# Performance work log

Measured on AMD Instinct MI355X. Metric: run time of the kernel, lower is better.

Reference implementation:

```python
import jax, jax.numpy as jnp
import numpy as np


def _lstm_layer(x, w_ih, w_hh, b_ih, b_hh):
    """Single LSTM layer, batch_first x: [B, T, D] -> [B, T, H]. Gate order i,f,g,o."""
    B, T, _ = x.shape
    H = w_hh.shape[1]
    # Precompute input-to-gates for all timesteps: [B, T, 4H]
    xg = jnp.einsum('btd,gd->btg', x, w_ih) + b_ih + b_hh

    def step(carry, xg_t):
        h, c = carry
        g = xg_t + h @ w_hh.T  # [B, 4H]
        i, f, gg, o = jnp.split(g, 4, axis=-1)
        i = jax.nn.sigmoid(i)
        f = jax.nn.sigmoid(f)
        gg = jnp.tanh(gg)
        o = jax.nn.sigmoid(o)
        c = f * c + i * gg
        h = o * jnp.tanh(c)
        return (h, c), h

    h0 = jnp.zeros((B, H), x.dtype)
    (_, _), hs = jax.lax.scan(step, (h0, h0), jnp.swapaxes(xg, 0, 1))
    return jnp.swapaxes(hs, 0, 1)  # [B, T, H]


def setup_inputs() -> dict:
    key = jax.random.key(0)
    ks = jax.random.split(key, 11)
    B, T, E, H = 128, 512, 256, 512
    s_e = 1.0 / np.sqrt(H)
    inp = {
        'x': jax.random.normal(ks[0], (B, T, E), jnp.float32),
        'w_ih0': jax.random.uniform(ks[1], (4 * H, E), jnp.float32, -s_e, s_e),
        'w_hh0': jax.random.uniform(ks[2], (4 * H, H), jnp.float32, -s_e, s_e),
        'b_ih0': jax.random.uniform(ks[3], (4 * H,), jnp.float32, -s_e, s_e),
        'b_hh0': jax.random.uniform(ks[4], (4 * H,), jnp.float32, -s_e, s_e),
        'w_ih1': jax.random.uniform(ks[5], (4 * H, H), jnp.float32, -s_e, s_e),
        'w_hh1': jax.random.uniform(ks[6], (4 * H, H), jnp.float32, -s_e, s_e),
        'b_ih1': jax.random.uniform(ks[7], (4 * H,), jnp.float32, -s_e, s_e),
        'b_hh1': jax.random.uniform(ks[8], (4 * H,), jnp.float32, -s_e, s_e),
        'w_fc': jax.random.uniform(ks[9], (1, H), jnp.float32, -s_e, s_e),
        'b_fc': jax.random.uniform(ks[10], (1,), jnp.float32, -s_e, s_e),
    }
    return inp


def reference(x, w_ih0, w_hh0, b_ih0, b_hh0, w_ih1, w_hh1, b_ih1, b_hh1, w_fc, b_fc):
    h1 = _lstm_layer(x, w_ih0, w_hh0, b_ih0, b_hh0)   # [B, T, H]
    h2 = _lstm_layer(h1, w_ih1, w_hh1, b_ih1, b_hh1)  # [B, T, H]
    last = h2[:, -1, :]                               # [B, H]
    out = last @ w_fc.T + b_fc                        # [B, 1]
    return jax.nn.sigmoid(out)
```

## Files before the change

kernel.cpp:

```cpp
#include <hip/hip_runtime.h>

using u16    = unsigned short;
using u64_t  = unsigned long long;
using short4v = __attribute__((ext_vector_type(4))) short;
using short8 = __attribute__((ext_vector_type(8))) short;
using f32x4  = __attribute__((ext_vector_type(4))) float;

#define T_STEPS 512
#define BATCH   128
#define HDIM    512
#define EDIM    256
#define NWG     256
#define WGS     256
#define HPITCH  65536

__device__ __forceinline__ u16 f2bf(float f) {
  unsigned u = __float_as_uint(f);
  u += 0x7FFFu + ((u >> 16) & 1u);
  return (u16)(u >> 16);
}
__device__ __forceinline__ float bf2f(u16 h) {
  return __uint_as_float(((unsigned)h) << 16);
}
__device__ __forceinline__ float sigm(float x) { return 1.0f / (1.0f + __expf(-x)); }
__device__ __forceinline__ float ftanh(float x) { return 1.0f - 2.0f / (__expf(2.0f * x) + 1.0f); }

__device__ __forceinline__ u64_t cl8(const u16* p) {
  return __hip_atomic_load((const u64_t*)p, __ATOMIC_RELAXED, __HIP_MEMORY_SCOPE_AGENT);
}
__device__ __forceinline__ void cstore2(u16* p, u16 v) {
  __hip_atomic_store(p, v, __ATOMIC_RELAXED, __HIP_MEMORY_SCOPE_AGENT);
}
__device__ __forceinline__ int ld4(const int* p) {
  return __hip_atomic_load(p, __ATOMIC_RELAXED, __HIP_MEMORY_SCOPE_AGENT);
}
__device__ __forceinline__ short8 mk8(u64_t lo, u64_t hi) {
  short4v a = __builtin_bit_cast(short4v, lo);
  short4v b = __builtin_bit_cast(short4v, hi);
  return __builtin_shufflevector(a, b, 0, 1, 2, 3, 4, 5, 6, 7);
}

__global__ void cvt_bf16_kernel(const float* __restrict__ src, u16* __restrict__ dst, int n4) {
  int i = blockIdx.x * blockDim.x + threadIdx.x;
  if (i >= n4) return;
  float4 v = ((const float4*)src)[i];
  uint2 o;
  o.x = (unsigned)f2bf(v.x) | ((unsigned)f2bf(v.y) << 16);
  o.y = (unsigned)f2bf(v.z) | ((unsigned)f2bf(v.w) << 16);
  ((uint2*)dst)[i] = o;
}


__device__ __forceinline__ void grid_barrier(int* cnt, int* root, int* rel,
                                             int it, int tid, int bid) {
  __syncthreads();
  if (tid == 0) {
    int* mycnt = cnt + (bid >> 5) * 64;
    int old = __hip_atomic_fetch_add(mycnt, 1, __ATOMIC_RELAXED, __HIP_MEMORY_SCOPE_AGENT);
    if (old == 32 * (it + 1) - 1) {
      int r = __hip_atomic_fetch_add(root, 1, __ATOMIC_RELAXED, __HIP_MEMORY_SCOPE_AGENT);
      if (r == 8 * (it + 1) - 1)
        __hip_atomic_store(rel, it + 1, __ATOMIC_RELAXED, __HIP_MEMORY_SCOPE_AGENT);
    }
    while (__hip_atomic_load(rel, __ATOMIC_RELAXED, __HIP_MEMORY_SCOPE_AGENT) < it + 1)
      __builtin_amdgcn_s_sleep(1);
  }
  __syncthreads();
}

__global__ void __launch_bounds__(WGS, 1) lstm_kernel(
    const float* __restrict__ wih0, const float* __restrict__ whh0,
    const float* __restrict__ bih0, const float* __restrict__ bhh0,
    const float* __restrict__ wih1, const float* __restrict__ whh1,
    const float* __restrict__ bih1, const float* __restrict__ bhh1,
    const float* __restrict__ wfc,  const float* __restrict__ bfc,
    const u16* __restrict__ xbf, u16* __restrict__ h0buf, u16* __restrict__ h1buf,
    float* __restrict__ out, int* syncp, int hist)
{
  extern __shared__ u16 smem[];
  u16* Ws_in  = smem;
  u16* Ws_rec = smem + 16384;

  const int tid    = threadIdx.x;
  const int bid    = blockIdx.x;
  const int layer  = bid >> 7;
  const int lb     = bid & 127;
  const int mhalf  = lb & 1;
  const int nc     = lb >> 1;
  const int jbase  = nc * 8;
  const int w      = tid >> 6;
  const int lane   = tid & 63;
  const int l15    = lane & 15;
  const int q      = lane >> 4;
  const int wmbase = mhalf * 64 + w * 16;
  const int gid    = layer * 2 + mhalf;

  char* sb = (char*)syncp;

  const int K_in = layer ? HDIM : EDIM;
  const float* Wih = layer ? wih1 : wih0;
  const float* Whh = layer ? whh1 : whh0;
  const float* Bih = layer ? bih1 : bih0;
  const float* Bhh = layer ? bhh1 : bhh0;

  for (int p = tid; p < 32 * (K_in / 8); p += WGS) {
    int c = p >> 5, n = p & 31;
    int grow = (n >> 3) * HDIM + jbase + (n & 7);
    const float* s = Wih + (size_t)grow * K_in + c * 8;
    u16* d = Ws_in + p * 8;
    #pragma unroll
    for (int e = 0; e < 8; ++e) d[e] = f2bf(s[e]);
  }
  for (int p = tid; p < 32 * (HDIM / 8); p += WGS) {
    int c = p >> 5, n = p & 31;
    int grow = (n >> 3) * HDIM + jbase + (n & 7);
    const float* s = Whh + (size_t)grow * HDIM + c * 8;
    u16* d = Ws_rec + p * 8;
    #pragma unroll
    for (int e = 0; e < 8; ++e) d[e] = f2bf(s[e]);
  }

  const int cc = l15 & 7;
  const float bi_i = Bih[0*HDIM + jbase + cc] + Bhh[0*HDIM + jbase + cc];
  const float bi_f = Bih[1*HDIM + jbase + cc] + Bhh[1*HDIM + jbase + cc];
  const float bi_g = Bih[2*HDIM + jbase + cc] + Bhh[2*HDIM + jbase + cc];
  const float bi_o = Bih[3*HDIM + jbase + cc] + Bhh[3*HDIM + jbase + cc];

  __syncthreads();

  float cst[4] = {0.f, 0.f, 0.f, 0.f};
  u16* ownbuf = layer ? h1buf : h0buf;
  const int arow = wmbase + l15;
  const size_t cbase = ((size_t)q * 128 + arow) * 8;

  auto MM2 = [&](short8 a, const u16* Ws, int kk, f32x4& A0, f32x4& A1) {
    const u16* bb = Ws + (kk * 4 + q) * 256 + l15 * 8;
    short8 b0 = *(const short8*)bb;
    short8 b1 = *(const short8*)(bb + 128);
    A0 = __builtin_amdgcn_mfma_f32_16x16x32_bf16(a, b0, A0, 0, 0, 0);
    A1 = __builtin_amdgcn_mfma_f32_16x16x32_bf16(a, b1, A1, 0, 0, 0);
  };

  if (hist) {
    const int* own_rel = (const int*)(sb + 20480 + (size_t)(gid * 8 + (nc >> 3)) * 256);
    const int* l0_rel  = (const int*)(sb + 20480 + (size_t)(mhalf * 8 + (nc >> 3)) * 256);
    int* sub_cnt = (int*)(sb + (size_t)gid * 4096 + (size_t)(nc >> 3) * 256);
    int* root_cnt = (int*)(sb + 16384 + (size_t)gid * 256);

    for (int t = 0; t < T_STEPS; ++t) {
      short8 xfr[8];
      if (layer == 0) {
        const u16* xb = xbf + ((size_t)arow * T_STEPS + t) * EDIM + q * 8;
        #pragma unroll
        for (int kk = 0; kk < 8; ++kk) xfr[kk] = *(const short8*)(xb + kk * 32);
      }

      if (tid == 0) {
        if (layer == 0) {
          if (t > 0) while (ld4(own_rel) < t) {}
        } else {
          while (ld4(own_rel) < t || ld4(l0_rel) < t + 1) {}
        }
      }
      __syncthreads();

      short8 ifr[16];
      short8 rfr[16];
      if (layer == 1) {
        const u16* ab = h0buf + (size_t)t * HPITCH + cbase;
        #pragma unroll
        for (int kk = 0; kk < 16; ++kk) ifr[kk] = *(const short8*)(ab + kk * 4096);
      }
      if (t > 0) {
        const u16* rb = ownbuf + (size_t)(t - 1) * HPITCH + cbase;
        #pragma unroll
        for (int kk = 0; kk < 16; ++kk) rfr[kk] = *(const short8*)(rb + kk * 4096);
      }

      f32x4 a0A = {0,0,0,0}, a1A = {0,0,0,0}, a0B = {0,0,0,0}, a1B = {0,0,0,0};
      if (layer == 0) {
        #pragma unroll
        for (int kk = 0; kk < 8; ++kk)
          MM2(xfr[kk], Ws_in, kk, (kk & 1) ? a0B : a0A, (kk & 1) ? a1B : a1A);
      } else {
        #pragma unroll
        for (int kk = 0; kk < 16; ++kk)
          MM2(ifr[kk], Ws_in, kk, (kk & 1) ? a0B : a0A, (kk & 1) ? a1B : a1A);
      }
      if (t > 0) {
        #pragma unroll
        for (int kk = 0; kk < 16; ++kk)
          MM2(rfr[kk], Ws_rec, kk, (kk & 1) ? a0B : a0A, (kk & 1) ? a1B : a1A);
      }
      f32x4 acc0 = a0A + a0B;
      f32x4 acc1 = a1A + a1B;

      u16* hw = ownbuf + (size_t)t * HPITCH + (size_t)nc * 1024;
      const bool low = (l15 < 8);
      #pragma unroll
      for (int r = 0; r < 4; ++r) {
        float a0 = acc0[r], a1 = acc1[r];
        float p0 = __shfl_xor(a0, 8);
        float p1 = __shfl_xor(a1, 8);
        float iv = low ? a0 : p0;
        float fv = low ? p0 : a0;
        float gv = low ? a1 : p1;
        float ov = low ? p1 : a1;
        iv = sigm(iv + bi_i);
        fv = sigm(fv + bi_f);
        gv = ftanh(gv + bi_g);
        ov = sigm(ov + bi_o);
        float cn = fv * cst[r] + iv * gv;
        cst[r] = cn;
        float hv = ov * ftanh(cn);
        if (low) cstore2(&hw[(size_t)(wmbase + q * 4 + r) * 8 + cc], f2bf(hv));
      }

      __syncthreads();
      if (tid == 0) {
        int old = __hip_atomic_fetch_add(sub_cnt, 1, __ATOMIC_RELAXED, __HIP_MEMORY_SCOPE_AGENT);
        if (old == 8 * (t + 1) - 1) {
          int r = __hip_atomic_fetch_add(root_cnt, 1, __ATOMIC_RELAXED, __HIP_MEMORY_SCOPE_AGENT);
          if (r == 8 * (t + 1) - 1) {
            #pragma unroll
            for (int l = 0; l < 8; ++l)
              __hip_atomic_store((int*)(sb + 20480 + (size_t)(gid * 8 + l) * 256), t + 1,
                                 __ATOMIC_RELAXED, __HIP_MEMORY_SCOPE_AGENT);
          }
        }
      }
    }

    if (bid == NWG - 1) {
      const int* g2 = (const int*)(sb + 20480 + (size_t)(2 * 8 + 0) * 256);
      const int* g3 = (const int*)(sb + 20480 + (size_t)(3 * 8 + 0) * 256);
      if (tid == 0) { while (ld4(g2) < T_STEPS || ld4(g3) < T_STEPS) {} }
      __syncthreads();
      __builtin_amdgcn_fence(__ATOMIC_ACQUIRE, "agent");
      const int b = tid >> 1, half = tid & 1;
      const u16* hp = h1buf + (size_t)(T_STEPS - 1) * HPITCH;
      const float* wf = wfc + half * 256;
      float s = 0.f;
      for (int cg = 0; cg < 32; ++cg) {
        const u16* p = hp + ((size_t)(half * 32 + cg) * 128 + b) * 8;
        #pragma unroll
        for (int e = 0; e < 8; ++e) s += bf2f(p[e]) * wf[cg * 8 + e];
      }
      s += __shfl_xor(s, 1);
      if (half == 0) out[b] = sigm(s + bfc[0]);
    }
    return;
  }

  int* f_cnt  = (int*)(sb + 28672);
  int* f_root = (int*)(sb + 30720);
  int* f_rel  = (int*)(sb + 30848);
  for (int it = 0; it <= T_STEPS; ++it) {
    const int t = layer ? (it - 1) : it;
    if (t >= 0 && t < T_STEPS) {
      short8 ifr[16];
      short8 rfr[16];
      short8 xfr[8];
      if (layer == 1) {
        const u16* ab = h0buf + (size_t)(t & 1) * HPITCH + cbase;
        #pragma unroll
        for (int kk = 0; kk < 16; ++kk)
          ifr[kk] = mk8(cl8(ab + kk * 4096), cl8(ab + kk * 4096 + 4));
      }
      if (t > 0) {
        const u16* rb = ownbuf + (size_t)((t - 1) & 1) * HPITCH + cbase;
        #pragma unroll
        for (int kk = 0; kk < 16; ++kk)
          rfr[kk] = mk8(cl8(rb + kk * 4096), cl8(rb + kk * 4096 + 4));
      }
      if (layer == 0) {
        const u16* xb = xbf + ((size_t)arow * T_STEPS + t) * EDIM + q * 8;
        #pragma unroll
        for (int kk = 0; kk < 8; ++kk) xfr[kk] = *(const short8*)(xb + kk * 32);
      }

      f32x4 a0A = {0,0,0,0}, a1A = {0,0,0,0}, a0B = {0,0,0,0}, a1B = {0,0,0,0};
      if (layer == 0) {
        #pragma unroll
        for (int kk = 0; kk < 8; ++kk)
          MM2(xfr[kk], Ws_in, kk, (kk & 1) ? a0B : a0A, (kk & 1) ? a1B : a1A);
      } else {
        #pragma unroll
        for (int kk = 0; kk < 16; ++kk)
          MM2(ifr[kk], Ws_in, kk, (kk & 1) ? a0B : a0A, (kk & 1) ? a1B : a1A);
      }
      if (t > 0) {
        #pragma unroll
        for (int kk = 0; kk < 16; ++kk)
          MM2(rfr[kk], Ws_rec, kk, (kk & 1) ? a0B : a0A, (kk & 1) ? a1B : a1A);
      }
      f32x4 acc0 = a0A + a0B;
      f32x4 acc1 = a1A + a1B;

      u16* hw = ownbuf + (size_t)(t & 1) * HPITCH + (size_t)nc * 1024;
      const bool low = (l15 < 8);
      #pragma unroll
      for (int r = 0; r < 4; ++r) {
        float a0 = acc0[r], a1 = acc1[r];
        float p0 = __shfl_xor(a0, 8);
        float p1 = __shfl_xor(a1, 8);
        float iv = low ? a0 : p0;
        float fv = low ? p0 : a0;
        float gv = low ? a1 : p1;
        float ov = low ? p1 : a1;
        iv = sigm(iv + bi_i);
        fv = sigm(fv + bi_f);
        gv = ftanh(gv + bi_g);
        ov = sigm(ov + bi_o);
        float cn = fv * cst[r] + iv * gv;
        cst[r] = cn;
        float hv = ov * ftanh(cn);
        if (low) cstore2(&hw[(size_t)(wmbase + q * 4 + r) * 8 + cc], f2bf(hv));
      }
    }
    grid_barrier(f_cnt, f_root, f_rel, it, tid, bid);
  }
  if (bid == NWG - 1) {
    __builtin_amdgcn_fence(__ATOMIC_ACQUIRE, "agent");
    const int b = tid >> 1, half = tid & 1;
    const u16* hp = h1buf + (size_t)1 * HPITCH;
    const float* wf = wfc + half * 256;
    float s = 0.f;
    for (int cg = 0; cg < 32; ++cg) {
      const u16* p = hp + ((size_t)(half * 32 + cg) * 128 + b) * 8;
      #pragma unroll
      for (int e = 0; e < 8; ++e) s += bf2f(p[e]) * wf[cg * 8 + e];
    }
    s += __shfl_xor(s, 1);
    if (half == 0) out[b] = sigm(s + bfc[0]);
  }
}

extern "C" void kernel_launch(void* const* d_in, const int* in_sizes, int n_in,
                              void* d_out, int out_size, void* d_ws, size_t ws_size,
                              hipStream_t stream) {
  (void)in_sizes; (void)n_in; (void)out_size;
  const float* x    = (const float*)d_in[0];
  const float* wih0 = (const float*)d_in[1];
  const float* whh0 = (const float*)d_in[2];
  const float* bih0 = (const float*)d_in[3];
  const float* bhh0 = (const float*)d_in[4];
  const float* wih1 = (const float*)d_in[5];
  const float* whh1 = (const float*)d_in[6];
  const float* bih1 = (const float*)d_in[7];
  const float* bhh1 = (const float*)d_in[8];
  const float* wfc  = (const float*)d_in[9];
  const float* bfc  = (const float*)d_in[10];
  float* outp = (float*)d_out;

  char* ws = (char*)d_ws;
  int*  syncp = (int*)ws;
  u16*  xbf   = (u16*)(ws + 32768);
  u16*  h0    = (u16*)(ws + 32768 + 33554432);

  const size_t need_hist = 32768ull + 33554432ull + 2ull * T_STEPS * HPITCH * sizeof(u16);
  const int hist = (ws_size >= need_hist) ? 1 : 0;
  const size_t slots = hist ? T_STEPS : 2;
  u16* h1 = h0 + slots * HPITCH;

  hipMemsetAsync(d_ws, 0, 32768, stream);

  const int n4 = (BATCH * T_STEPS * EDIM) / 4;
  cvt_bf16_kernel<<<n4 / 256, 256, 0, stream>>>(x, xbf, n4);

  hipFuncSetAttribute((const void*)lstm_kernel,
                      hipFuncAttributeMaxDynamicSharedMemorySize, 65536);

  void* args[] = { (void*)&wih0, (void*)&whh0, (void*)&bih0, (void*)&bhh0,
                   (void*)&wih1, (void*)&whh1, (void*)&bih1, (void*)&bhh1,
                   (void*)&wfc,  (void*)&bfc,
                   (void*)&xbf,  (void*)&h0,   (void*)&h1,
                   (void*)&outp, (void*)&syncp, (void*)&hist };
  hipLaunchCooperativeKernel((void*)lstm_kernel, dim3(NWG), dim3(WGS),
                             args, 65536, stream);
}
```

Before: 2.399 ms.

## Replace hierarchical atomic counter barrier with per-block stamp polling by wavefront

Replaces the two-level fetch-add counter tree and release flags with per-workgroup timestamp slots: each block writes its step number into its own slot, and consumers poll all 64 slots of a group in parallel with one wavefront using __all. This removes serialized atomic read-modify-writes and the extra release-propagation hop from the per-timestep dependency chain. It adds a vmcnt(0) wait before the stamp store and increases polling traffic across a wavefront, and relocates the sync buffer offsets.

```diff
diff --git a/kernel.cpp b/kernel.cpp
--- a/kernel.cpp
+++ b/kernel.cpp
@@ -31,8 +31,14 @@
 __device__ __forceinline__ void cstore2(u16* p, u16 v) {
   __hip_atomic_store(p, v, __ATOMIC_RELAXED, __HIP_MEMORY_SCOPE_AGENT);
 }
+__device__ __forceinline__ void cstore4(int* p, int v) {
+  __hip_atomic_store(p, v, __ATOMIC_RELAXED, __HIP_MEMORY_SCOPE_AGENT);
+}
 __device__ __forceinline__ int ld4(const int* p) {
   return __hip_atomic_load(p, __ATOMIC_RELAXED, __HIP_MEMORY_SCOPE_AGENT);
+}
+__device__ __forceinline__ int addag(int* p, int v) {
+  return __hip_atomic_fetch_add(p, v, __ATOMIC_RELAXED, __HIP_MEMORY_SCOPE_AGENT);
 }
 __device__ __forceinline__ short8 mk8(u64_t lo, u64_t hi) {
   short4v a = __builtin_bit_cast(short4v, lo);
@@ -56,14 +62,12 @@
   __syncthreads();
   if (tid == 0) {
     int* mycnt = cnt + (bid >> 5) * 64;
-    int old = __hip_atomic_fetch_add(mycnt, 1, __ATOMIC_RELAXED, __HIP_MEMORY_SCOPE_AGENT);
+    int old = addag(mycnt, 1);
     if (old == 32 * (it + 1) - 1) {
-      int r = __hip_atomic_fetch_add(root, 1, __ATOMIC_RELAXED, __HIP_MEMORY_SCOPE_AGENT);
-      if (r == 8 * (it + 1) - 1)
-        __hip_atomic_store(rel, it + 1, __ATOMIC_RELAXED, __HIP_MEMORY_SCOPE_AGENT);
-    }
-    while (__hip_atomic_load(rel, __ATOMIC_RELAXED, __HIP_MEMORY_SCOPE_AGENT) < it + 1)
-      __builtin_amdgcn_s_sleep(1);
+      int r = addag(root, 1);
+      if (r == 8 * (it + 1) - 1) cstore4(rel, it + 1);
+    }
+    while (ld4(rel) < it + 1) __builtin_amdgcn_s_sleep(1);
   }
   __syncthreads();
 }
@@ -142,10 +146,9 @@
   };
 
   if (hist) {
-    const int* own_rel = (const int*)(sb + 20480 + (size_t)(gid * 8 + (nc >> 3)) * 256);
-    const int* l0_rel  = (const int*)(sb + 20480 + (size_t)(mhalf * 8 + (nc >> 3)) * 256);
-    int* sub_cnt = (int*)(sb + (size_t)gid * 4096 + (size_t)(nc >> 3) * 256);
-    int* root_cnt = (int*)(sb + 16384 + (size_t)gid * 256);
+    int* my_stamp = (int*)(sb + 4096 + (size_t)gid * 256 + (size_t)nc * 4);
+    const int* own_st = (const int*)(sb + 4096 + (size_t)gid * 256);
+    const int* l0_st  = (const int*)(sb + 4096 + (size_t)mhalf * 256);
 
     for (int t = 0; t < T_STEPS; ++t) {
       short8 xfr[8];
@@ -155,11 +158,17 @@
         for (int kk = 0; kk < 8; ++kk) xfr[kk] = *(const short8*)(xb + kk * 32);
       }
 
-      if (tid == 0) {
+      if (w == 0) {
         if (layer == 0) {
-          if (t > 0) while (ld4(own_rel) < t) {}
+          if (t > 0) {
+            for (;;) { int s = ld4(own_st + lane); if (__all(s >= t)) break; }
+          }
         } else {
-          while (ld4(own_rel) < t || ld4(l0_rel) < t + 1) {}
+          for (;;) {
+            int s  = ld4(own_st + lane);
+            int s0 = ld4(l0_st + lane);
+            if (__all((s >= t) && (s0 >= t + 1))) break;
+          }
         }
       }
       __syncthreads();
@@ -216,25 +225,21 @@
         if (low) cstore2(&hw[(size_t)(wmbase + q * 4 + r) * 8 + cc], f2bf(hv));
       }
 
+      asm volatile("s_waitcnt vmcnt(0)" ::: "memory");
       __syncthreads();
-      if (tid == 0) {
-        int old = __hip_atomic_fetch_add(sub_cnt, 1, __ATOMIC_RELAXED, __HIP_MEMORY_SCOPE_AGENT);
-        if (old == 8 * (t + 1) - 1) {
-          int r = __hip_atomic_fetch_add(root_cnt, 1, __ATOMIC_RELAXED, __HIP_MEMORY_SCOPE_AGENT);
-          if (r == 8 * (t + 1) - 1) {
-            #pragma unroll
-            for (int l = 0; l < 8; ++l)
-              __hip_atomic_store((int*)(sb + 20480 + (size_t)(gid * 8 + l) * 256), t + 1,
-                                 __ATOMIC_RELAXED, __HIP_MEMORY_SCOPE_AGENT);
-          }
+      if (tid == 0) cstore4(my_stamp, t + 1);
+    }
+
+    if (bid == NWG - 1) {
+      const int* g2 = (const int*)(sb + 4096 + (size_t)2 * 256);
+      const int* g3 = (const int*)(sb + 4096 + (size_t)3 * 256);
+      if (w == 0) {
+        for (;;) {
+          int a = ld4(g2 + lane);
+          int b = ld4(g3 + lane);
+          if (__all((a >= T_STEPS) && (b >= T_STEPS))) break;
         }
       }
-    }
-
-    if (bid == NWG - 1) {
-      const int* g2 = (const int*)(sb + 20480 + (size_t)(2 * 8 + 0) * 256);
-      const int* g3 = (const int*)(sb + 20480 + (size_t)(3 * 8 + 0) * 256);
-      if (tid == 0) { while (ld4(g2) < T_STEPS || ld4(g3) < T_STEPS) {} }
       __syncthreads();
       __builtin_amdgcn_fence(__ATOMIC_ACQUIRE, "agent");
       const int b = tid >> 1, half = tid & 1;
@@ -252,9 +257,9 @@
     return;
   }
 
-  int* f_cnt  = (int*)(sb + 28672);
-  int* f_root = (int*)(sb + 30720);
-  int* f_rel  = (int*)(sb + 30848);
+  int* f_cnt  = (int*)(sb + 8192);
+  int* f_root = (int*)(sb + 10240);
+  int* f_rel  = (int*)(sb + 10368);
   for (int it = 0; it <= T_STEPS; ++it) {
     const int t = layer ? (it - 1) : it;
     if (t >= 0 && t < T_STEPS) {
```

New measurement: 2.982 ms. +24.3%, slower.
